# Kernel optimization log

Hardware: AMD Instinct MI355X
Metric: run time of the kernel (lower is better)

The kernel has to match this reference:

```python
import jax, jax.numpy as jnp
import numpy as np

CONF_THRES = 0.25
IOU_THRES = 0.45
MAX_DET = 300
MAX_WH = 4096.0  # class offset for class-aware (non-agnostic) NMS
B, N, NC = 16, 25200, 80


def setup_inputs() -> dict:
    key = jax.random.key(0)
    k1, k2 = jax.random.split(key)
    p = jax.random.uniform(k1, (B, N, 5 + NC), dtype=jnp.float32)
    # scale to realistic YOLO pixel-space xywh for a 640x640 image
    cx = p[..., 0] * 640.0
    cy = p[..., 1] * 640.0
    w = p[..., 2] * 96.0 + 4.0
    h = p[..., 3] * 96.0 + 4.0
    obj = p[..., 4]
    cls = p[..., 5:] * 0.9
    prediction = jnp.concatenate([jnp.stack([cx, cy, w, h, obj], axis=-1), cls], axis=-1)
    logits = jax.random.normal(k2, (B, N, NC), dtype=jnp.float32)
    return {"prediction": prediction, "logits": logits}


def xywh2xyxy(b):
    cx, cy, w, h = b[..., 0], b[..., 1], b[..., 2], b[..., 3]
    return jnp.stack([cx - w * 0.5, cy - h * 0.5, cx + w * 0.5, cy + h * 0.5], axis=-1)


def _iou_one_vs_all(box, boxes):
    # box: [4], boxes: [N,4] in xyxy
    lt = jnp.maximum(box[:2], boxes[:, :2])
    rb = jnp.minimum(box[2:], boxes[:, 2:])
    wh = jnp.clip(rb - lt, 0.0)
    inter = wh[:, 0] * wh[:, 1]
    a1 = (box[2] - box[0]) * (box[3] - box[1])
    a2 = (boxes[:, 2] - boxes[:, 0]) * (boxes[:, 3] - boxes[:, 1])
    return inter / (a1 + a2 - inter + 1e-9)


def _nms_image(x6, boxes_off, scores, log_):
    # greedy NMS, fixed MAX_DET iterations; suppressed/invalid scores are -1
    def step(s, _):
        best = jnp.argmax(s)
        keep = s[best] > 0.0
        iou = _iou_one_vs_all(boxes_off[best], boxes_off)
        s = jnp.where(iou > IOU_THRES, -1.0, s)  # also suppresses 'best' (IoU=1)
        return s, (best, keep)
    _, (idx, keep) = jax.lax.scan(step, scores, None, length=MAX_DET)
    km = keep.astype(x6.dtype)[:, None]
    dets = x6[idx] * km          # [MAX_DET, 6] zero-padded
    lg = log_[idx] * km          # [MAX_DET, 80]
    return dets, lg, keep


def reference(prediction, logits):
    obj = prediction[..., 4]                          # [B,N]
    cls_conf = prediction[..., 5:] * obj[..., None]   # x[:,5:] *= x[:,4:5]
    conf = jnp.max(cls_conf, axis=-1)                 # best class conf
    j = jnp.argmax(cls_conf, axis=-1)                 # best class index
    box = xywh2xyxy(prediction[..., :4])              # [B,N,4]
    valid = (obj > CONF_THRES) & (conf > CONF_THRES)
    scores = jnp.where(valid, conf, -1.0)
    boxes_off = box + (j.astype(box.dtype) * MAX_WH)[..., None]  # class-aware offset
    x6 = jnp.concatenate([box, conf[..., None], j.astype(box.dtype)[..., None]], axis=-1)
    dets, lg, keep = jax.vmap(_nms_image)(x6, boxes_off, scores, logits)
    return dets, lg, keep
```

## Files before the change

kernel.cpp:

```cpp
#include <hip/hip_runtime.h>
#include <cstdint>

#define BB 16
#define NN 25200
#define NCLS 80
#define ROW 85
#define MAXDET 300
#define HBINS 2048
#define CAP2 512
#define TGT 448
#define CONF_T 0.25f
#define IOU_T 0.45f
#define NT 1024

static const size_t OFF_KEYS  = 1612800;
static const size_t OFF_CBOX  = OFF_KEYS  + 65536;
static const size_t OFF_RAW   = OFF_CBOX  + 131072;
static const size_t OFF_CCLS  = OFF_RAW   + 131072;
static const size_t OFF_CCNT  = OFF_CCLS  + 32768;
static const size_t OFF_MASK  = OFF_CCNT  + 64;
static const size_t OFF_MASKT = OFF_MASK  + 524288;

__global__ __launch_bounds__(256) void k_pre(const float* __restrict__ pred,
                                             float* __restrict__ scoreArr) {
    int tid = threadIdx.x;
    int t = tid & 3;
    int row = blockIdx.x * 64 + (tid >> 2);
    const float* rp = pred + (size_t)row * ROW;
    int start = (t == 0) ? 0 : (1 + 21 * t);
    int cnt   = (t == 0) ? 22 : 21;
    float obj = rp[4];
    float best = -1.0f; int bc = 1 << 20;
#pragma unroll
    for (int k = 0; k < 22; ++k) {
        if (k < cnt) {
            int col = start + k;
            if (col >= 5) {
                float v = __fmul_rn(rp[col], obj);
                if (v > best) { best = v; bc = col; }
            }
        }
    }
#pragma unroll
    for (int d = 1; d <= 2; d <<= 1) {
        float ob = __shfl_xor(best, d);
        int   oc = __shfl_xor(bc, d);
        if (ob > best || (ob == best && oc < bc)) { best = ob; bc = oc; }
    }
    if (t == 0) {
        bool valid = (obj > CONF_T) && (best > CONF_T);
        scoreArr[row] = valid ? best : -1.0f;
    }
}

__global__ __launch_bounds__(NT) void k_sel(const float* __restrict__ pred,
                                            const float* __restrict__ scoreArr,
                                            unsigned long long* __restrict__ keysG,
                                            float4* __restrict__ cboxG,
                                            float4* __restrict__ rawG,
                                            unsigned* __restrict__ cclsG,
                                            int* __restrict__ ccnt) {
    __shared__ unsigned hist[HBINS];
    __shared__ unsigned csum[257];
    __shared__ unsigned long long keys[CAP2];
    __shared__ int flags[2];

    int b = blockIdx.x, tid = threadIdx.x;
    int lane = tid & 63;

    for (int k = tid; k < HBINS; k += NT) hist[k] = 0u;
    if (tid == 0) { flags[0] = 0; flags[1] = 0; }
    __syncthreads();

    float sreg[25];
#pragma unroll
    for (int t = 0; t < 25; ++t) {
        int n = tid + t * NT;
        float s = (n < NN) ? scoreArr[(size_t)b * NN + n] : -1.0f;
        sreg[t] = s;
        if (s > 0.0f) {
            unsigned key = (__float_as_uint(s) - 0x3E800000u) >> 13;
            if (key > HBINS - 1) key = HBINS - 1;
            atomicAdd(&hist[key], 1u);
        }
    }
    __syncthreads();

    if (tid < 256) {
        unsigned cs = 0;
#pragma unroll
        for (int t = 0; t < 8; ++t) cs += hist[tid * 8 + t];
        csum[tid] = cs;
    }
    __syncthreads();
    for (int off = 1; off < 256; off <<= 1) {
        unsigned v = 0, add = 0;
        if (tid < 256) {
            v = csum[tid];
            add = (tid + off < 256) ? csum[tid + off] : 0u;
        }
        __syncthreads();
        if (tid < 256) csum[tid] = v + add;
        __syncthreads();
    }
    if (tid < 256) {
        unsigned Sc = csum[tid];
        unsigned Sn = (tid < 255) ? csum[tid + 1] : 0u;
        if (Sc >= TGT && (tid == 255 || Sn < TGT)) {
            unsigned cum = Sn;
            int t = tid * 8;
            for (int k = tid * 8 + 7; k >= tid * 8; --k) {
                cum += hist[k];
                if (cum >= TGT) { t = k; break; }
            }
            flags[1] = t;
        }
    }
    __syncthreads();
    unsigned thr = (unsigned)flags[1];

#pragma unroll
    for (int t = 0; t < 25; ++t) {
        int n = tid + t * NT;
        float s = sreg[t];
        bool win = false;
        if (s > 0.0f) {
            unsigned key = (__float_as_uint(s) - 0x3E800000u) >> 13;
            if (key > HBINS - 1) key = HBINS - 1;
            win = (key >= thr);
        }
        unsigned long long m = __ballot(win);
        if (m) {
            int lead = __ffsll((long long)m) - 1;
            int base = 0;
            if (lane == lead) base = atomicAdd(&flags[0], __popcll(m));
            base = __shfl(base, lead);
            if (win) {
                int pos = base + __popcll(m & ((1ULL << lane) - 1ULL));
                if (pos < CAP2)
                    keys[pos] = ((unsigned long long)__float_as_uint(s) << 32)
                              | (unsigned long long)(0xFFFFFFFFu - (unsigned)n);
            }
        }
    }
    __syncthreads();
    int c = min(flags[0], CAP2);
    for (int p = tid; p < CAP2; p += NT)
        if (p >= c) keys[p] = 0ULL;
    __syncthreads();

    for (int k = 2; k <= CAP2; k <<= 1) {
        for (int j = k >> 1; j > 0; j >>= 1) {
            for (int i = tid; i < CAP2; i += NT) {
                int ixj = i ^ j;
                if (ixj > i) {
                    unsigned long long k1 = keys[i], k2 = keys[ixj];
                    bool sw = ((i & k) == 0) ? (k1 < k2) : (k1 > k2);
                    if (sw) { keys[i] = k2; keys[ixj] = k1; }
                }
            }
            __syncthreads();
        }
    }

    if (tid < CAP2) {
        int p = tid;
        if (p < c) {
            int n = (int)(0xFFFFFFFFu - (unsigned)keys[p]);
            const float* rp = pred + ((size_t)b * NN + n) * ROW;
            float cx = rp[0], cy = rp[1], w = rp[2], h = rp[3], obj = rp[4];
            float best = __fmul_rn(rp[5], obj);
            int bj = 0;
#pragma unroll 8
            for (int cc = 1; cc < NCLS; ++cc) {
                float v = __fmul_rn(rp[5 + cc], obj);
                if (v > best) { best = v; bj = cc; }
            }
            float hw = __fmul_rn(w, 0.5f), hh = __fmul_rn(h, 0.5f);
            float4 bb = make_float4(__fsub_rn(cx, hw), __fsub_rn(cy, hh),
                                    __fadd_rn(cx, hw), __fadd_rn(cy, hh));
            rawG[b * CAP2 + p] = bb;
            float off = __fmul_rn((float)bj, 4096.0f);
            cboxG[b * CAP2 + p] = make_float4(__fadd_rn(bb.x, off), __fadd_rn(bb.y, off),
                                              __fadd_rn(bb.z, off), __fadd_rn(bb.w, off));
            cclsG[b * CAP2 + p] = (unsigned)bj;
        } else {
            rawG[b * CAP2 + p]  = make_float4(0.f, 0.f, 0.f, 0.f);
            cboxG[b * CAP2 + p] = make_float4(0.f, 0.f, 0.f, 0.f);
            cclsG[b * CAP2 + p] = 0u;
        }
        keysG[b * CAP2 + p] = keys[p];
    }
    if (tid == 0) ccnt[b] = c;
}

__global__ __launch_bounds__(256) void k_mask(const float4* __restrict__ cboxG,
                                              const int* __restrict__ ccnt,
                                              unsigned long long* __restrict__ maskG,
                                              unsigned long long* __restrict__ maskTG) {
    __shared__ float4 cb[CAP2];
    int b = blockIdx.x >> 3, w = blockIdx.x & 7;
    int tid = threadIdx.x;
    cb[tid] = cboxG[b * CAP2 + tid];
    cb[256 + tid] = cboxG[b * CAP2 + 256 + tid];
    __syncthreads();
    int c = min(ccnt[b], CAP2);
    int jbase = w << 6;
    for (int i = tid; i < CAP2; i += 256) {
        unsigned long long m = 0ULL;
        if (i < c && i < jbase + 63) {
            float4 ci = cb[i];
            float a1 = __fmul_rn(__fsub_rn(ci.z, ci.x), __fsub_rn(ci.w, ci.y));
#pragma unroll 4
            for (int jj = 0; jj < 64; ++jj) {
                int j = jbase + jj;
                float4 cj = cb[j];
                float ltx = fmaxf(ci.x, cj.x), lty = fmaxf(ci.y, cj.y);
                float rbx = fminf(ci.z, cj.z), rby = fminf(ci.w, cj.w);
                float ww = fmaxf(__fsub_rn(rbx, ltx), 0.0f);
                float hh = fmaxf(__fsub_rn(rby, lty), 0.0f);
                float inter = __fmul_rn(ww, hh);
                if (j > i && inter > 0.0f) {
                    float a2 = __fmul_rn(__fsub_rn(cj.z, cj.x), __fsub_rn(cj.w, cj.y));
                    float denom = __fadd_rn(__fsub_rn(__fadd_rn(a1, a2), inter), 1e-9f);
                    if (inter / denom > IOU_T) m |= (1ULL << jj);
                }
            }
        }
        maskG[((size_t)(b * CAP2 + i)) * 8 + w] = m;
    }
    if (tid < 64) {
        int l = tid, p = jbase + l;
        unsigned long long m = 0ULL;
        if (p < c) {
            float4 cl = cb[p];
            float a2 = __fmul_rn(__fsub_rn(cl.z, cl.x), __fsub_rn(cl.w, cl.y));
            for (int ii = 0; ii < 64; ++ii) {
                float4 ci = cb[jbase + ii];
                float ltx = fmaxf(ci.x, cl.x), lty = fmaxf(ci.y, cl.y);
                float rbx = fminf(ci.z, cl.z), rby = fminf(ci.w, cl.w);
                float ww = fmaxf(__fsub_rn(rbx, ltx), 0.0f);
                float hh = fmaxf(__fsub_rn(rby, lty), 0.0f);
                float inter = __fmul_rn(ww, hh);
                if (ii < l && inter > 0.0f) {
                    float a1 = __fmul_rn(__fsub_rn(ci.z, ci.x), __fsub_rn(ci.w, ci.y));
                    float denom = __fadd_rn(__fsub_rn(__fadd_rn(a1, a2), inter), 1e-9f);
                    if (inter / denom > IOU_T) m |= (1ULL << ii);
                }
            }
        }
        maskTG[((size_t)(b * 8 + w)) * 64 + l] = m;
    }
}

__global__ __launch_bounds__(NT) void k_fin(const float* __restrict__ logits,
                                            const unsigned long long* __restrict__ keysG,
                                            const float4* __restrict__ rawG,
                                            const unsigned* __restrict__ cclsG,
                                            const int* __restrict__ ccnt,
                                            const unsigned long long* __restrict__ maskG,
                                            const unsigned long long* __restrict__ maskTG,
                                            float* __restrict__ out) {
    __shared__ unsigned long long keepm_s[8];
    __shared__ unsigned kidx[64];
    __shared__ unsigned rowsrc_s[MAXDET];
    __shared__ int s_kept;

    int b = blockIdx.x, tid = threadIdx.x;
    int c = min(ccnt[b], CAP2);

    if (tid < 64) {
        int lane = tid;
        unsigned long long remq = 0ULL;
        int kept = 0;
        for (int w = 0; w < 8; ++w) {
            int base = w << 6;
            unsigned long long tw = __shfl(remq, w);
            bool pre = ((tw >> lane) & 1ULL) != 0ULL;
            bool validl = (base + lane) < c;
            unsigned long long Cl = maskTG[((size_t)(b * 8 + w)) * 64 + lane];
            unsigned long long initK = __ballot(validl && !pre);
            unsigned long long K = initK;
            for (int it = 0; it < 64; ++it) {
                bool sup = (Cl & K & ((1ULL << lane) - 1ULL)) != 0ULL;
                unsigned long long K2 = initK & __ballot(!sup);
                if (K2 == K) break;
                K = K2;
            }
            int limit = MAXDET - kept;
            int nk = __popcll(K);
            if (nk > limit) {
                if (limit <= 0) K = 0ULL;
                else {
                    int pref = __popcll(K & ((2ULL << lane) - 1ULL));
                    bool el = ((K >> lane) & 1ULL) && (pref <= limit);
                    K = __ballot(el);
                }
            }
            kept += __popcll(K);
            if (lane == 0) keepm_s[w] = K;
            if (K != 0ULL && w < 7) {
                if ((K >> lane) & 1ULL) {
                    int r = __popcll(K & ((1ULL << lane) - 1ULL));
                    kidx[r] = (unsigned)lane;
                }
                __builtin_amdgcn_s_waitcnt(0);
                int nkk = __popcll(K);
                int q = lane & 7, slot = lane >> 3;
                unsigned long long acc = 0ULL;
                for (int t = slot; t < nkk; t += 8)
                    acc |= maskG[((size_t)(b * CAP2 + base + (int)kidx[t])) * 8 + q];
                acc |= __shfl_xor(acc, 8);
                acc |= __shfl_xor(acc, 16);
                acc |= __shfl_xor(acc, 32);
                if (slot == 0) remq |= acc;
            }
        }
        if (lane == 0) s_kept = kept;
    }
    __syncthreads();
    int kept = s_kept;

    float* dets = out;
    float* lg   = out + (size_t)BB * MAXDET * 6;
    float* kpo  = lg  + (size_t)BB * MAXDET * NCLS;

    for (int p = tid; p < CAP2; p += NT) {
        if (p < c) {
            int w = p >> 6, bitp = p & 63;
            unsigned long long kw = keepm_s[w];
            if ((kw >> bitp) & 1ULL) {
                int rank = __popcll(kw & ((1ULL << bitp) - 1ULL));
                for (int q = 0; q < w; ++q) rank += __popcll(keepm_s[q]);
                if (rank < MAXDET) {
                    float4 bb = rawG[b * CAP2 + p];
                    unsigned long long key = keysG[b * CAP2 + p];
                    float* dr = dets + ((size_t)b * MAXDET + rank) * 6;
                    dr[0] = bb.x; dr[1] = bb.y; dr[2] = bb.z; dr[3] = bb.w;
                    dr[4] = __uint_as_float((unsigned)(key >> 32));
                    dr[5] = (float)cclsG[b * CAP2 + p];
                    rowsrc_s[rank] = 0xFFFFFFFFu - (unsigned)key;
                }
            }
        }
    }
    for (int i = tid; i < MAXDET; i += NT) {
        if (i >= kept) {
            float* dr = dets + ((size_t)b * MAXDET + i) * 6;
#pragma unroll
            for (int q = 0; q < 6; ++q) dr[q] = 0.0f;
        }
        kpo[b * MAXDET + i] = (i < kept) ? 1.0f : 0.0f;
    }
    __syncthreads();
    for (int i = tid; i < MAXDET * NCLS; i += NT) {
        int t = i / NCLS, col = i - t * NCLS;
        float v = 0.0f;
        if (t < kept) v = logits[((size_t)b * NN + rowsrc_s[t]) * NCLS + col];
        lg[(size_t)b * MAXDET * NCLS + i] = v;
    }
}

extern "C" void kernel_launch(void* const* d_in, const int* in_sizes, int n_in,
                              void* d_out, int out_size, void* d_ws, size_t ws_size,
                              hipStream_t stream) {
    const float* pred   = (const float*)d_in[0];
    const float* logits = (const float*)d_in[1];
    float* out = (float*)d_out;
    char* ws = (char*)d_ws;

    float* scr = (float*)ws;
    unsigned long long* keysG  = (unsigned long long*)(ws + OFF_KEYS);
    float4* cboxG              = (float4*)(ws + OFF_CBOX);
    float4* rawG               = (float4*)(ws + OFF_RAW);
    unsigned* cclsG            = (unsigned*)(ws + OFF_CCLS);
    int* ccnt                  = (int*)(ws + OFF_CCNT);
    unsigned long long* maskG  = (unsigned long long*)(ws + OFF_MASK);
    unsigned long long* maskTG = (unsigned long long*)(ws + OFF_MASKT);

    k_pre<<<6300, 256, 0, stream>>>(pred, scr);
    k_sel<<<BB, NT, 0, stream>>>(pred, scr, keysG, cboxG, rawG, cclsG, ccnt);
    k_mask<<<BB * 8, 256, 0, stream>>>(cboxG, ccnt, maskG, maskTG);
    k_fin<<<BB, NT, 0, stream>>>(logits, keysG, rawG, cclsG, ccnt, maskG, maskTG, out);
}
```

Before: 346.4 us.

## Fuse select, IoU mask and final NMS into one per-image kernel using LDS

Merges the selection, IoU-mask and finalize kernels into a single 1024-thread block per image. Candidate boxes, keys, classes and both suppression masks now live in shared memory, with the histogram and mask arrays sharing storage through a union, so the global workspace round trips and two launches are gone. The mask work that used 128 blocks now runs on only 16 blocks, which cuts parallelism for that stage. Separately, k_pre now reads each prediction row with 4-wide vector loads.

```diff
diff --git a/kernel.cpp b/kernel.cpp
--- a/kernel.cpp
+++ b/kernel.cpp
@@ -13,13 +13,8 @@
 #define IOU_T 0.45f
 #define NT 1024
 
-static const size_t OFF_KEYS  = 1612800;
-static const size_t OFF_CBOX  = OFF_KEYS  + 65536;
-static const size_t OFF_RAW   = OFF_CBOX  + 131072;
-static const size_t OFF_CCLS  = OFF_RAW   + 131072;
-static const size_t OFF_CCNT  = OFF_CCLS  + 32768;
-static const size_t OFF_MASK  = OFF_CCNT  + 64;
-static const size_t OFF_MASKT = OFF_MASK  + 524288;
+typedef float f4u __attribute__((ext_vector_type(4), aligned(4)));
+
 
 __global__ __launch_bounds__(256) void k_pre(const float* __restrict__ pred,
                                              float* __restrict__ scoreArr) {
@@ -27,19 +22,27 @@
     int t = tid & 3;
     int row = blockIdx.x * 64 + (tid >> 2);
     const float* rp = pred + (size_t)row * ROW;
-    int start = (t == 0) ? 0 : (1 + 21 * t);
-    int cnt   = (t == 0) ? 22 : 21;
     float obj = rp[4];
     float best = -1.0f; int bc = 1 << 20;
 #pragma unroll
-    for (int k = 0; k < 22; ++k) {
-        if (k < cnt) {
-            int col = start + k;
-            if (col >= 5) {
-                float v = __fmul_rn(rp[col], obj);
-                if (v > best) { best = v; bc = col; }
-            }
-        }
+    for (int i = 0; i < 6; ++i) {
+        int jj = t + 4 * i;
+        if (jj < 21) {
+            f4u v4 = *reinterpret_cast<const f4u*>(rp + 4 * jj);
+            int c0 = 4 * jj;
+#pragma unroll
+            for (int e = 0; e < 4; ++e) {
+                int col = c0 + e;
+                if (col >= 5) {
+                    float v = __fmul_rn(v4[e], obj);
+                    if (v > best) { best = v; bc = col; }
+                }
+            }
+        }
+    }
+    if (t == 1) {
+        float v = __fmul_rn(rp[84], obj);
+        if (v > best) { best = v; bc = 84; }
     }
 #pragma unroll
     for (int d = 1; d <= 2; d <<= 1) {
@@ -53,22 +56,29 @@
     }
 }
 
-__global__ __launch_bounds__(NT) void k_sel(const float* __restrict__ pred,
-                                            const float* __restrict__ scoreArr,
-                                            unsigned long long* __restrict__ keysG,
-                                            float4* __restrict__ cboxG,
-                                            float4* __restrict__ rawG,
-                                            unsigned* __restrict__ cclsG,
-                                            int* __restrict__ ccnt) {
-    __shared__ unsigned hist[HBINS];
-    __shared__ unsigned csum[257];
+__global__ __launch_bounds__(NT) void k_fused(const float* __restrict__ pred,
+                                              const float* __restrict__ scoreArr,
+                                              const float* __restrict__ logits,
+                                              float* __restrict__ out) {
+    __shared__ union {
+        struct { unsigned hist[HBINS]; unsigned csum[257]; } h;
+        unsigned long long maskS[CAP2][8];
+    } u;
     __shared__ unsigned long long keys[CAP2];
+    __shared__ float4 cbox_s[CAP2];
+    __shared__ float4 raw_s[CAP2];
+    __shared__ unsigned ccls_s[CAP2];
+    __shared__ unsigned long long maskT_s[8][64];
+    __shared__ unsigned long long keepm_s[8];
+    __shared__ unsigned kidx[64];
+    __shared__ unsigned rowsrc_s[MAXDET];
     __shared__ int flags[2];
+    __shared__ int s_kept;
 
     int b = blockIdx.x, tid = threadIdx.x;
     int lane = tid & 63;
 
-    for (int k = tid; k < HBINS; k += NT) hist[k] = 0u;
+    for (int k = tid; k < HBINS; k += NT) u.h.hist[k] = 0u;
     if (tid == 0) { flags[0] = 0; flags[1] = 0; }
     __syncthreads();
 
@@ -81,7 +91,7 @@
         if (s > 0.0f) {
             unsigned key = (__float_as_uint(s) - 0x3E800000u) >> 13;
             if (key > HBINS - 1) key = HBINS - 1;
-            atomicAdd(&hist[key], 1u);
+            atomicAdd(&u.h.hist[key], 1u);
         }
     }
     __syncthreads();
@@ -89,28 +99,28 @@
     if (tid < 256) {
         unsigned cs = 0;
 #pragma unroll
-        for (int t = 0; t < 8; ++t) cs += hist[tid * 8 + t];
-        csum[tid] = cs;
+        for (int t = 0; t < 8; ++t) cs += u.h.hist[tid * 8 + t];
+        u.h.csum[tid] = cs;
     }
     __syncthreads();
     for (int off = 1; off < 256; off <<= 1) {
         unsigned v = 0, add = 0;
         if (tid < 256) {
-            v = csum[tid];
-            add = (tid + off < 256) ? csum[tid + off] : 0u;
+            v = u.h.csum[tid];
+            add = (tid + off < 256) ? u.h.csum[tid + off] : 0u;
         }
         __syncthreads();
-        if (tid < 256) csum[tid] = v + add;
+        if (tid < 256) u.h.csum[tid] = v + add;
         __syncthreads();
     }
     if (tid < 256) {
-        unsigned Sc = csum[tid];
-        unsigned Sn = (tid < 255) ? csum[tid + 1] : 0u;
+        unsigned Sc = u.h.csum[tid];
+        unsigned Sn = (tid < 255) ? u.h.csum[tid + 1] : 0u;
         if (Sc >= TGT && (tid == 255 || Sn < TGT)) {
             unsigned cum = Sn;
             int t = tid * 8;
             for (int k = tid * 8 + 7; k >= tid * 8; --k) {
-                cum += hist[k];
+                cum += u.h.hist[k];
                 if (cum >= TGT) { t = k; break; }
             }
             flags[1] = t;
@@ -179,42 +189,31 @@
             float hw = __fmul_rn(w, 0.5f), hh = __fmul_rn(h, 0.5f);
             float4 bb = make_float4(__fsub_rn(cx, hw), __fsub_rn(cy, hh),
                                     __fadd_rn(cx, hw), __fadd_rn(cy, hh));
-            rawG[b * CAP2 + p] = bb;
+            raw_s[p] = bb;
             float off = __fmul_rn((float)bj, 4096.0f);
-            cboxG[b * CAP2 + p] = make_float4(__fadd_rn(bb.x, off), __fadd_rn(bb.y, off),
-                                              __fadd_rn(bb.z, off), __fadd_rn(bb.w, off));
-            cclsG[b * CAP2 + p] = (unsigned)bj;
+            cbox_s[p] = make_float4(__fadd_rn(bb.x, off), __fadd_rn(bb.y, off),
+                                    __fadd_rn(bb.z, off), __fadd_rn(bb.w, off));
+            ccls_s[p] = (unsigned)bj;
         } else {
-            rawG[b * CAP2 + p]  = make_float4(0.f, 0.f, 0.f, 0.f);
-            cboxG[b * CAP2 + p] = make_float4(0.f, 0.f, 0.f, 0.f);
-            cclsG[b * CAP2 + p] = 0u;
-        }
-        keysG[b * CAP2 + p] = keys[p];
-    }
-    if (tid == 0) ccnt[b] = c;
-}
-
-__global__ __launch_bounds__(256) void k_mask(const float4* __restrict__ cboxG,
-                                              const int* __restrict__ ccnt,
-                                              unsigned long long* __restrict__ maskG,
-                                              unsigned long long* __restrict__ maskTG) {
-    __shared__ float4 cb[CAP2];
-    int b = blockIdx.x >> 3, w = blockIdx.x & 7;
-    int tid = threadIdx.x;
-    cb[tid] = cboxG[b * CAP2 + tid];
-    cb[256 + tid] = cboxG[b * CAP2 + 256 + tid];
-    __syncthreads();
-    int c = min(ccnt[b], CAP2);
-    int jbase = w << 6;
-    for (int i = tid; i < CAP2; i += 256) {
+            raw_s[p]  = make_float4(0.f, 0.f, 0.f, 0.f);
+            cbox_s[p] = make_float4(0.f, 0.f, 0.f, 0.f);
+            ccls_s[p] = 0u;
+        }
+    }
+    __syncthreads();
+
+    for (int k = tid; k < CAP2 * 8; k += NT) {
+        int i = k & (CAP2 - 1);
+        int w = k >> 9;
+        int jbase = w << 6;
         unsigned long long m = 0ULL;
         if (i < c && i < jbase + 63) {
-            float4 ci = cb[i];
+            float4 ci = cbox_s[i];
             float a1 = __fmul_rn(__fsub_rn(ci.z, ci.x), __fsub_rn(ci.w, ci.y));
 #pragma unroll 4
             for (int jj = 0; jj < 64; ++jj) {
                 int j = jbase + jj;
-                float4 cj = cb[j];
+                float4 cj = cbox_s[j];
                 float ltx = fmaxf(ci.x, cj.x), lty = fmaxf(ci.y, cj.y);
                 float rbx = fminf(ci.z, cj.z), rby = fminf(ci.w, cj.w);
                 float ww = fmaxf(__fsub_rn(rbx, ltx), 0.0f);
@@ -227,16 +226,17 @@
                 }
             }
         }
-        maskG[((size_t)(b * CAP2 + i)) * 8 + w] = m;
-    }
-    if (tid < 64) {
-        int l = tid, p = jbase + l;
+        u.maskS[i][w] = m;
+    }
+    if (tid < 512) {
+        int w = tid >> 6, l = tid & 63;
+        int jbase = w << 6, p = jbase + l;
         unsigned long long m = 0ULL;
         if (p < c) {
-            float4 cl = cb[p];
+            float4 cl = cbox_s[p];
             float a2 = __fmul_rn(__fsub_rn(cl.z, cl.x), __fsub_rn(cl.w, cl.y));
             for (int ii = 0; ii < 64; ++ii) {
-                float4 ci = cb[jbase + ii];
+                float4 ci = cbox_s[jbase + ii];
                 float ltx = fmaxf(ci.x, cl.x), lty = fmaxf(ci.y, cl.y);
                 float rbx = fminf(ci.z, cl.z), rby = fminf(ci.w, cl.w);
                 float ww = fmaxf(__fsub_rn(rbx, ltx), 0.0f);
@@ -249,28 +249,11 @@
                 }
             }
         }
-        maskTG[((size_t)(b * 8 + w)) * 64 + l] = m;
-    }
-}
-
-__global__ __launch_bounds__(NT) void k_fin(const float* __restrict__ logits,
-                                            const unsigned long long* __restrict__ keysG,
-                                            const float4* __restrict__ rawG,
-                                            const unsigned* __restrict__ cclsG,
-                                            const int* __restrict__ ccnt,
-                                            const unsigned long long* __restrict__ maskG,
-                                            const unsigned long long* __restrict__ maskTG,
-                                            float* __restrict__ out) {
-    __shared__ unsigned long long keepm_s[8];
-    __shared__ unsigned kidx[64];
-    __shared__ unsigned rowsrc_s[MAXDET];
-    __shared__ int s_kept;
-
-    int b = blockIdx.x, tid = threadIdx.x;
-    int c = min(ccnt[b], CAP2);
+        maskT_s[w][l] = m;
+    }
+    __syncthreads();
 
     if (tid < 64) {
-        int lane = tid;
         unsigned long long remq = 0ULL;
         int kept = 0;
         for (int w = 0; w < 8; ++w) {
@@ -278,7 +261,7 @@
             unsigned long long tw = __shfl(remq, w);
             bool pre = ((tw >> lane) & 1ULL) != 0ULL;
             bool validl = (base + lane) < c;
-            unsigned long long Cl = maskTG[((size_t)(b * 8 + w)) * 64 + lane];
+            unsigned long long Cl = maskT_s[w][lane];
             unsigned long long initK = __ballot(validl && !pre);
             unsigned long long K = initK;
             for (int it = 0; it < 64; ++it) {
@@ -309,7 +292,7 @@
                 int q = lane & 7, slot = lane >> 3;
                 unsigned long long acc = 0ULL;
                 for (int t = slot; t < nkk; t += 8)
-                    acc |= maskG[((size_t)(b * CAP2 + base + (int)kidx[t])) * 8 + q];
+                    acc |= u.maskS[base + (int)kidx[t]][q];
                 acc |= __shfl_xor(acc, 8);
                 acc |= __shfl_xor(acc, 16);
                 acc |= __shfl_xor(acc, 32);
@@ -333,12 +316,12 @@
                 int rank = __popcll(kw & ((1ULL << bitp) - 1ULL));
                 for (int q = 0; q < w; ++q) rank += __popcll(keepm_s[q]);
                 if (rank < MAXDET) {
-                    float4 bb = rawG[b * CAP2 + p];
-                    unsigned long long key = keysG[b * CAP2 + p];
+                    float4 bb = raw_s[p];
+                    unsigned long long key = keys[p];
                     float* dr = dets + ((size_t)b * MAXDET + rank) * 6;
                     dr[0] = bb.x; dr[1] = bb.y; dr[2] = bb.z; dr[3] = bb.w;
                     dr[4] = __uint_as_float((unsigned)(key >> 32));
-                    dr[5] = (float)cclsG[b * CAP2 + p];
+                    dr[5] = (float)ccls_s[p];
                     rowsrc_s[rank] = 0xFFFFFFFFu - (unsigned)key;
                 }
             }
@@ -367,19 +350,8 @@
     const float* pred   = (const float*)d_in[0];
     const float* logits = (const float*)d_in[1];
     float* out = (float*)d_out;
-    char* ws = (char*)d_ws;
-
-    float* scr = (float*)ws;
-    unsigned long long* keysG  = (unsigned long long*)(ws + OFF_KEYS);
-    float4* cboxG              = (float4*)(ws + OFF_CBOX);
-    float4* rawG               = (float4*)(ws + OFF_RAW);
-    unsigned* cclsG            = (unsigned*)(ws + OFF_CCLS);
-    int* ccnt                  = (int*)(ws + OFF_CCNT);
-    unsigned long long* maskG  = (unsigned long long*)(ws + OFF_MASK);
-    unsigned long long* maskTG = (unsigned long long*)(ws + OFF_MASKT);
+    float* scr = (float*)d_ws;
 
     k_pre<<<6300, 256, 0, stream>>>(pred, scr);
-    k_sel<<<BB, NT, 0, stream>>>(pred, scr, keysG, cboxG, rawG, cclsG, ccnt);
-    k_mask<<<BB * 8, 256, 0, stream>>>(cboxG, ccnt, maskG, maskTG);
-    k_fin<<<BB, NT, 0, stream>>>(logits, keysG, rawG, cclsG, ccnt, maskG, maskTG, out);
+    k_fused<<<BB, NT, 0, stream>>>(pred, scr, logits, out);
 }
```

After: 320.4 us. 7.5% less time.
